# Kernel tuning notes

Measured on AMD Instinct MI355X. Metric: run time of the kernel, lower is better.

Reference implementation:

```python
import jax, jax.numpy as jnp
import numpy as np

B, N, F_IN, F_OUT, K = 128, 400, 128, 128, 5


def setup_inputs() -> dict:
    key = jax.random.key(0)
    ks = jax.random.split(key, 7)
    s_in = 1.0 / np.sqrt(F_IN)
    s_out = 1.0 / np.sqrt(F_OUT)
    return {
        "x": jax.random.normal(ks[0], (B, N, F_IN), dtype=jnp.float32),
        # SAGEConv layer 1: lin_l (neighbor agg, with bias) and lin_r (root, no bias)
        "W1l": jax.random.normal(ks[1], (F_OUT, F_IN), dtype=jnp.float32) * s_in,
        "b1l": jnp.zeros((F_OUT,), dtype=jnp.float32),
        "W1r": jax.random.normal(ks[2], (F_OUT, F_IN), dtype=jnp.float32) * s_in,
        # SAGEConv layer 2
        "W2l": jax.random.normal(ks[3], (F_OUT, F_OUT), dtype=jnp.float32) * s_out,
        "b2l": jnp.zeros((F_OUT,), dtype=jnp.float32),
        "W2r": jax.random.normal(ks[4], (F_OUT, F_OUT), dtype=jnp.float32) * s_out,
    }


def _knn_sym_adj(x):
    # x: [B, N, F]. Per-batch 5-NN graph with self-loops (loop=True),
    # then symmetrized (to_undirected coalesces duplicates -> 0/1 adjacency).
    sq = jnp.sum(x * x, axis=-1)                       # [B, N]
    d2 = sq[:, :, None] + sq[:, None, :] - 2.0 * jnp.einsum("bnd,bmd->bnm", x, x)
    _, idx = jax.lax.top_k(-d2, K)                     # [B, N, K] nearest incl. self
    A = jnp.zeros((x.shape[0], x.shape[1], x.shape[1]), dtype=x.dtype)
    bi = jnp.arange(x.shape[0])[:, None, None]
    ni = jnp.arange(x.shape[1])[None, :, None]
    A = A.at[bi, ni, idx].set(1.0)                     # A[b,i,j]=1 if j in knn(i)
    return jnp.maximum(A, A.transpose(0, 2, 1))        # undirected


def _sage(h, A, deg, Wl, bl, Wr):
    # PyG SAGEConv (mean aggr): out = lin_l(mean_j x_j) + lin_r(x_i)
    m = jnp.einsum("bnm,bmf->bnf", A, h) / deg
    return m @ Wl.T + bl + h @ Wr.T


def reference(x, W1l, b1l, W1r, W2l, b2l, W2r):
    A = _knn_sym_adj(x)
    deg = jnp.sum(A, axis=-1, keepdims=True)           # >=1 (self-loop)
    h = jax.nn.relu(_sage(x, A, deg, W1l, b1l, W1r))
    h = _sage(h, A, deg, W2l, b2l, W2r)
    return h.reshape(B * N, F_OUT)
```

## Files before the change

### kernel.cpp

```cpp
#include <hip/hip_runtime.h>
#include <hip/hip_bf16.h>
#include <stdint.h>

#define B_   128
#define N_   400
#define F_   128
#define K_   5
#define ROWS (B_ * N_)
#define POOLCAP 2048
#define DCAP 416
#define MAXFLAG ROWS
#define GAP_HEDGE 5e-4
#define DELTA_MAX 0.18f
#define NW 13
#define NCAND 24

typedef __attribute__((ext_vector_type(8))) short bf16x8;
typedef __attribute__((ext_vector_type(4))) float f32x4;

static __device__ __forceinline__ unsigned short f2bf(float f) {
  union { float f; unsigned u; } v; v.f = f;
  unsigned r = v.u + 0x7fff + ((v.u >> 16) & 1);
  return (unsigned short)(r >> 16);
}
static __device__ __forceinline__ float bf2f(unsigned short h) {
  union { unsigned u; float f; } v; v.u = ((unsigned)h) << 16; return v.f;
}

template<int M, typename T>
static __device__ __forceinline__ void insM(T d, int j, T bd[], int bj[]) {
  if (d < bd[M - 1] || (d == bd[M - 1] && j < bj[M - 1])) {
    bd[M - 1] = d; bj[M - 1] = j;
#pragma unroll
    for (int q = M - 1; q > 0; --q) {
      bool sw = (bd[q] < bd[q - 1]) || (bd[q] == bd[q - 1] && bj[q] < bj[q - 1]);
      T td = bd[q]; int tj = bj[q];
      if (sw) { bd[q] = bd[q - 1]; bd[q - 1] = td; bj[q] = bj[q - 1]; bj[q - 1] = tj; }
    }
  }
}

__global__ __launch_bounds__(256) void k_prep_rows(const float* __restrict__ x,
                                                   unsigned short* __restrict__ Y,
                                                   float* __restrict__ sq) {
  int wave = threadIdx.x >> 6, lane = threadIdx.x & 63;
  int row = blockIdx.x * 4 + wave;
  float2 v = *(const float2*)&x[(size_t)row * F_ + lane * 2];
  unsigned short hx = f2bf(v.x), hy = f2bf(v.y);
  float lx = v.x - bf2f(hx), ly = v.y - bf2f(hy);
  *(unsigned*)&Y[(size_t)row * 256 + lane * 2]       = (unsigned)hx | ((unsigned)hy << 16);
  *(unsigned*)&Y[(size_t)row * 256 + 128 + lane * 2] = (unsigned)f2bf(lx) | ((unsigned)f2bf(ly) << 16);
  float s = v.x * v.x + v.y * v.y;
#pragma unroll
  for (int o = 32; o > 0; o >>= 1) s += __shfl_xor(s, o);
  if (lane == 0) sq[row] = s;
}

__global__ __launch_bounds__(256) void k_prep_w(const float* __restrict__ W1l,
                                                const float* __restrict__ W1r,
                                                const float* __restrict__ W2l,
                                                const float* __restrict__ W2r,
                                                unsigned short* __restrict__ Wh,
                                                unsigned short* __restrict__ Wlo) {
  int t = blockIdx.x * 256 + threadIdx.x;
  int m = t >> 14, e = t & 16383;
  const float* src = (m == 0) ? W1l : (m == 1) ? W1r : (m == 2) ? W2l : W2r;
  float f = src[e];
  unsigned short h = f2bf(f);
  Wh[t] = h;
  Wlo[t] = f2bf(f - bf2f(h));
}

#define YJ_STRIDE 264
__global__ __launch_bounds__(256) void k_knn(const unsigned short* __restrict__ Y,
                                             const float* __restrict__ sq,
                                             int* __restrict__ idxout,
                                             int* __restrict__ flagcnt,
                                             int* __restrict__ flagrows,
                                             int* __restrict__ cand) {
  __shared__ unsigned short Yj[64 * YJ_STRIDE];
  __shared__ float sqj[64];

  int b = blockIdx.y, i0 = blockIdx.x * 64;
  int tid = threadIdx.x, wave = tid >> 6, lane = tid & 63;

  int i_local = wave * 16 + (lane & 15);
  int arow = b * N_ + min(i0 + i_local, N_ - 1);
  float sqi = sq[arow];

  const bf16x8* abase = (const bf16x8*)&Y[(size_t)arow * 256];
  bf16x8 af[8];
#pragma unroll
  for (int kc = 0; kc < 8; ++kc) af[kc] = abase[kc * 4 + (lane >> 4)];

  float bd[6] = {3.4e38f, 3.4e38f, 3.4e38f, 3.4e38f, 3.4e38f, 3.4e38f};
  int   bj[6] = {1 << 30, 1 << 30, 1 << 30, 1 << 30, 1 << 30, 1 << 30};

  const float4* srcb = (const float4*)(Y + (size_t)b * N_ * 256);

  for (int jt = 0; jt < 7; ++jt) {
    int j0 = jt * 64;
    float4* dst4 = (float4*)Yj;
#pragma unroll
    for (int q = 0; q < 8; ++q) {
      int l = tid + 256 * q;
      int r = l >> 5, cc = l & 31;
      int jr = min(j0 + r, N_ - 1);
      dst4[r * 33 + cc] = srcb[jr * 32 + cc];
    }
    if (tid < 64) sqj[tid] = sq[b * N_ + min(j0 + tid, N_ - 1)];
    __syncthreads();

#pragma unroll
    for (int ct = 0; ct < 4; ++ct) {
      f32x4 acc = {0.f, 0.f, 0.f, 0.f};
      int jfr = ct * 16 + (lane & 15);
      const bf16x8* bbase = (const bf16x8*)&Yj[jfr * YJ_STRIDE];
#pragma unroll
      for (int kc = 0; kc < 12; ++kc) {
        int bidx = (kc & 3) * 4 + ((kc >= 8) ? 16 : 0) + (lane >> 4);
        acc = __builtin_amdgcn_mfma_f32_16x16x32_bf16(bbase[bidx], af[kc & 7], acc, 0, 0, 0);
      }
      int jbase = ct * 16 + (lane >> 4) * 4;
      float4 sjv = *(const float4*)&sqj[jbase];
      float sj4[4] = {sjv.x, sjv.y, sjv.z, sjv.w};
#pragma unroll
      for (int r = 0; r < 4; ++r) {
        int j = j0 + jbase + r;
        float d = sqi + sj4[r] - 2.0f * acc[r];
        if (j < N_) insM<6, float>(d, j, bd, bj);
      }
    }
    __syncthreads();
  }

  float* mbd = (float*)Yj;
  int*   mbj = (int*)Yj + 64 * 33;
  int slot = i_local * 33 + (lane >> 4) * 6;
#pragma unroll
  for (int q = 0; q < 6; ++q) { mbd[slot + q] = bd[q]; mbj[slot + q] = bj[q]; }
  __syncthreads();

  if (tid < 64) {
    int i = i0 + tid;
    if (i < N_) {
      float fd[6] = {3.4e38f, 3.4e38f, 3.4e38f, 3.4e38f, 3.4e38f, 3.4e38f};
      int   fj[6] = {1 << 30, 1 << 30, 1 << 30, 1 << 30, 1 << 30, 1 << 30};
      for (int q = 0; q < NCAND; ++q)
        insM<6, float>(mbd[tid * 33 + q], mbj[tid * 33 + q], fd, fj);
      int gi = b * N_ + i;
#pragma unroll
      for (int q = 0; q < 5; ++q) idxout[gi * K_ + q] = fj[q];
      if (fd[5] - fd[4] < 0.02f) {
        int pos = atomicAdd(flagcnt, 1);
        if (pos < MAXFLAG) {
          flagrows[pos] = gi;
          for (int q = 0; q < NCAND; ++q) cand[gi * 32 + q] = mbj[tid * 33 + q];
        }
      }
    }
  }
}

__global__ __launch_bounds__(256) void k_refine(const float* __restrict__ x,
                                                const int* __restrict__ flagrows,
                                                const int* __restrict__ flagcnt,
                                                const int* __restrict__ cand,
                                                int* __restrict__ idx,
                                                int* __restrict__ hcnt,
                                                int* __restrict__ hrows,
                                                int* __restrict__ hab) {
  __shared__ double dbuf[8][32];
  __shared__ int    jbuf[8][32];
  int slot = threadIdx.x >> 5, c = threadIdx.x & 31;
  int nflag = min(*flagcnt, MAXFLAG);
  for (int base = blockIdx.x * 8; base < nflag; base += gridDim.x * 8) {
    int t = base + slot;
    __syncthreads();
    if (t < nflag) {
      if (c < NCAND) {
        int row = flagrows[t];
        int b = row / N_;
        int j = cand[row * 32 + c];
        const float* xi = x + (size_t)row * F_;
        const float* xj = x + (size_t)(b * N_ + j) * F_;
        double s = 0.0;
#pragma unroll
        for (int q = 0; q < 128; ++q) {
          double d = (double)xi[q] - (double)xj[q];
          s = fma(d, d, s);
        }
        dbuf[slot][c] = s; jbuf[slot][c] = j;
      } else {
        dbuf[slot][c] = 1e300; jbuf[slot][c] = 1 << 30;
      }
    }
    __syncthreads();
    if (c == 0 && t < nflag) {
      int row = flagrows[t];
      int b = row / N_;
      double fd[6] = {1e300, 1e300, 1e300, 1e300, 1e300, 1e300};
      int    fj[6] = {1 << 30, 1 << 30, 1 << 30, 1 << 30, 1 << 30, 1 << 30};
      for (int q = 0; q < NCAND; ++q) insM<6, double>(dbuf[slot][q], jbuf[slot][q], fd, fj);
#pragma unroll
      for (int q = 0; q < 5; ++q) idx[row * K_ + q] = fj[q];
      if (fd[5] - fd[4] < GAP_HEDGE) {
        int p = atomicAdd(hcnt, 1);
        if (p < MAXFLAG) {
          hrows[p] = row;
          hab[2 * p]     = b * N_ + fj[4];
          hab[2 * p + 1] = b * N_ + fj[5];
        }
      }
    }
  }
}

__global__ __launch_bounds__(512) void k_buildg(const int* __restrict__ idx,
                                                const int* __restrict__ c6,
                                                int* __restrict__ L6,
                                                float* __restrict__ W6,
                                                int* __restrict__ pooli,
                                                float* __restrict__ poolw,
                                                int* __restrict__ offi,
                                                int* __restrict__ cnti) {
  __shared__ unsigned bm1[N_][NW];
  __shared__ unsigned bmh[N_][NW];
  __shared__ int cs[512];
  int b = blockIdx.x, t = threadIdx.x;
  int gb0 = b * N_;

  for (int q = t; q < N_ * NW; q += 512) {
    (&bm1[0][0])[q] = 0u;
    (&bmh[0][0])[q] = 0u;
  }

  int i = t;
  int j0 = -1, j1 = -1, j2 = -1, j3 = -1, j4 = -1, y6 = -1;
  if (i < N_) {
    const int* ip = idx + (size_t)(gb0 + i) * 5;
    j0 = ip[0]; j1 = ip[1]; j2 = ip[2]; j3 = ip[3]; j4 = ip[4];
    y6 = c6[gb0 + i];
  }
  __syncthreads();

  if (i < N_) {
    unsigned bit = 1u << (i & 31);
    int w = i >> 5;
    if (j0 != i) atomicOr(&bm1[j0][w], bit);
    if (j1 != i) atomicOr(&bm1[j1][w], bit);
    if (j2 != i) atomicOr(&bm1[j2][w], bit);
    if (j3 != i) atomicOr(&bm1[j3][w], bit);
    if (j4 != i) {
      if (y6 >= 0) atomicOr(&bmh[j4][w], bit); else atomicOr(&bm1[j4][w], bit);
    }
    if (y6 >= 0 && y6 != i) atomicOr(&bmh[y6][w], bit);
  }
  __syncthreads();

  if (i < N_) {
    int gi = gb0 + i;
    int   jj[6]  = {j0, j1, j2, j3, j4, y6};
    float w1s[6] = {1.f, 1.f, 1.f, 1.f,
                    (y6 >= 0) ? 0.5f : 1.f,
                    (y6 >= 0) ? 0.5f : 0.f};
#pragma unroll
    for (int k = 0; k < 6; ++k) {
      int j = jj[k]; float w1 = w1s[k];
      size_t sl = (size_t)gi * 6 + k;
      if (w1 <= 0.f || j < 0) { L6[sl] = gi; W6[sl] = 0.f; continue; }
      if (j == i)             { L6[sl] = gi; W6[sl] = 1.f; continue; }
      float w2 = ((bm1[i][j >> 5] >> (j & 31)) & 1) ? 1.f
               : (((bmh[i][j >> 5] >> (j & 31)) & 1) ? 0.5f : 0.f);
      L6[sl] = gb0 + j; W6[sl] = fmaxf(w1, w2);
    }
  }

  unsigned mw[NW];
  int cnt_i = 0;
  if (i < N_) {
#pragma unroll
    for (int w = 0; w < NW; ++w) {
      unsigned ex = 0;
      if ((i  >> 5) == w) ex |= 1u << (i  & 31);
      if ((j0 >> 5) == w) ex |= 1u << (j0 & 31);
      if ((j1 >> 5) == w) ex |= 1u << (j1 & 31);
      if ((j2 >> 5) == w) ex |= 1u << (j2 & 31);
      if ((j3 >> 5) == w) ex |= 1u << (j3 & 31);
      if ((j4 >> 5) == w) ex |= 1u << (j4 & 31);
      if (y6 >= 0 && (y6 >> 5) == w) ex |= 1u << (y6 & 31);
      unsigned m = (bm1[i][w] | bmh[i][w]) & ~ex;
      mw[w] = m;
      cnt_i += __popc(m);
    }
  } else {
#pragma unroll
    for (int w = 0; w < NW; ++w) mw[w] = 0u;
  }

  cs[t] = (i < N_) ? cnt_i : 0;
  __syncthreads();
  for (int off = 1; off < 512; off <<= 1) {
    int v = (t >= off) ? cs[t - off] : 0;
    __syncthreads();
    cs[t] += v;
    __syncthreads();
  }

  if (i < N_) {
    int o = b * POOLCAP + cs[t] - cnt_i;
    offi[gb0 + i] = o;
    cnti[gb0 + i] = cnt_i;
    int c = 0;
#pragma unroll
    for (int w = 0; w < NW; ++w) {
      unsigned m = mw[w];
      unsigned ones = bm1[i][w];
      while (m) {
        int bit = __ffs(m) - 1; m &= m - 1;
        int r = w * 32 + bit;
        pooli[o + c] = gb0 + r;
        poolw[o + c] = ((ones >> bit) & 1) ? 1.f : 0.5f;
        ++c;
      }
    }
  }
}

__global__ __launch_bounds__(128) void k_delta(
    const float* __restrict__ P, const float* __restrict__ Qb,
    const float* __restrict__ b1, const unsigned short* __restrict__ h1b,
    const float* __restrict__ sumP, const float* __restrict__ degv,
    const int* __restrict__ L6, const float* __restrict__ W6,
    const int* __restrict__ pooli, const float* __restrict__ poolw,
    const int* __restrict__ offi, const int* __restrict__ cnti,
    const int* __restrict__ idx,
    const int* __restrict__ hcnt, const int* __restrict__ hrows,
    const int* __restrict__ hab,
    const float* __restrict__ W2l, const float* __restrict__ W2r,
    int* __restrict__ c6, int* __restrict__ dcnt, int* __restrict__ dlist) {
  __shared__ float H[3][2][128];
  __shared__ float dH[3][128];
  __shared__ float U[3][128];
  __shared__ float V1[128], V2[128], red[128];
  __shared__ float mU[3];
  __shared__ int   Ls[3][DCAP];
  __shared__ float Wsh[3][DCAP];
  int f = threadIdx.x;
  int n = min(*hcnt, MAXFLAG);
  for (int t = blockIdx.x; t < n; t += gridDim.x) {
    int gi = hrows[t], ga = hab[2 * t], gb = hab[2 * t + 1];
    int bb = gi / N_, iw = gi - bb * N_;
    bool ma = false, mb = false;
#pragma unroll
    for (int q = 0; q < K_; ++q) {
      ma = ma || (idx[ga * K_ + q] == iw);
      mb = mb || (idx[gb * K_ + q] == iw);
    }
    if (ma && mb) continue;
    int rows3[3] = {gi, ga, gb};
    int nn3[3];
    for (int s3 = 0; s3 < 3; ++s3) {
      int r = rows3[s3];
      int cc = cnti[r], oo = offi[r];
      int nn = 6 + cc; nn3[s3] = nn;
      for (int e = f; e < DCAP; e += 128) {
        int li = -1; float lw = 0.f;
        if (e < 6)      { li = L6[(size_t)r * 6 + e]; lw = W6[(size_t)r * 6 + e]; }
        else if (e < nn){ li = pooli[oo + e - 6];     lw = poolw[oo + e - 6]; }
        Ls[s3][e] = li; Wsh[s3][e] = lw;
      }
    }
    for (int s3 = 0; s3 < 3; ++s3) {
      int r = rows3[s3];
      float s1 = sumP[(size_t)r * 128 + f], d1 = degv[r];
      float ds = 0.f, dd = 0.f;
      if (s3 == 0) {
        if (!ma) { ds -= P[(size_t)ga * 128 + f]; dd -= 1.f; }
        if (!mb) { ds += P[(size_t)gb * 128 + f]; dd += 1.f; }
      } else if (s3 == 1) {
        if (!ma) { ds -= P[(size_t)gi * 128 + f]; dd -= 1.f; }
      } else {
        if (!mb) { ds += P[(size_t)gi * 128 + f]; dd += 1.f; }
      }
      float base = b1[f] + Qb[(size_t)r * 128 + f];
      float h0 = fmaxf(s1 / d1 + base, 0.f);
      float h1v = fmaxf((s1 + ds) / (d1 + dd) + base, 0.f);
      H[s3][0][f] = h0;
      H[s3][1][f] = h1v;
      dH[s3][f] = h1v - h0;
    }
    __syncthreads();
    {
      float u0 = 0.f, u1 = 0.f, u2 = 0.f;
      for (int f2 = 0; f2 < 128; ++f2) {
        float wv = W2l[f * 128 + f2];
        u0 += dH[0][f2] * wv;
        u1 += dH[1][f2] * wv;
        u2 += dH[2][f2] * wv;
      }
      U[0][f] = u0; U[1][f] = u1; U[2][f] = u2;
    }
    __syncthreads();
    red[f] = fabsf(U[0][f]);
    V1[f]  = fabsf(U[1][f]);
    V2[f]  = fabsf(U[2][f]);
    __syncthreads();
    for (int o = 64; o > 0; o >>= 1) {
      if (f < o) {
        red[f] = fmaxf(red[f], red[f + o]);
        V1[f]  = fmaxf(V1[f],  V1[f + o]);
        V2[f]  = fmaxf(V2[f],  V2[f + o]);
      }
      __syncthreads();
    }
    if (f == 0) { mU[0] = red[0]; mU[1] = V1[0]; mU[2] = V2[0]; }
    __syncthreads();
    float dmax = 0.f;
    for (int which = 0; which < 3; ++which) {
      float v1 = 0.f, v2 = 0.f;
      float d1r = degv[rows3[which]], d2r = d1r;
      int nnw = nn3[which];
      for (int e2 = 0; e2 < nnw; ++e2) {
        float w = Wsh[which][e2];
        if (w == 0.f) continue;
        int s = Ls[which][e2];
        float hv1, hv2;
        if (s == gi)      { hv1 = H[0][0][f]; hv2 = H[0][1][f]; }
        else if (s == ga) { hv1 = H[1][0][f]; hv2 = H[1][1][f]; }
        else if (s == gb) { hv1 = H[2][0][f]; hv2 = H[2][1][f]; }
        else {
          float hh = bf2f(h1b[(size_t)s * 256 + f]) + bf2f(h1b[(size_t)s * 256 + 128 + f]);
          hv1 = hh; hv2 = hh;
        }
        bool inG2 = true;
        if (which == 0 && s == ga && !ma) inG2 = false;
        if (which == 1 && s == gi && !ma) inG2 = false;
        v1 += w * hv1;
        if (inG2) v2 += w * hv2; else d2r -= w;
      }
      if (which == 0 && !mb) { v2 += H[2][1][f]; d2r += 1.f; }
      if (which == 2 && !mb) { v2 += H[0][1][f]; d2r += 1.f; }
      V1[f] = v1; V2[f] = v2;
      __syncthreads();
      float a1 = 0.f, a2 = 0.f, ow = 0.f;
      for (int f2 = 0; f2 < 128; ++f2) {
        float wl = W2l[f * 128 + f2];
        a1 += V1[f2] * wl;
        a2 += V2[f2] * wl;
        ow += dH[which][f2] * W2r[f * 128 + f2];
      }
      dmax = fmaxf(dmax, fabsf(a2 / d2r - a1 / d1r + ow));
      __syncthreads();
    }
    for (int li = 0; li < 3; ++li) {
      for (int e = f; e < nn3[li]; e += 128) {
        float w = Wsh[li][e];
        if (w == 0.f) continue;
        int r = Ls[li][e];
        if (r == gi || r == ga || r == gb) continue;
        bool dup = false;
        for (int lj = 0; lj < li && !dup; ++lj)
          for (int e2 = 0; e2 < nn3[lj]; ++e2)
            if (Ls[lj][e2] == r && Wsh[lj][e2] != 0.f) { dup = true; break; }
        if (dup) continue;
        float wi = 0.f, wa = 0.f, wb = 0.f;
        if (li == 0) wi = w; else if (li == 1) wa = w; else wb = w;
        int nz = 1;
        for (int lj = li + 1; lj < 3; ++lj)
          for (int e2 = 0; e2 < nn3[lj]; ++e2)
            if (Ls[lj][e2] == r && Wsh[lj][e2] != 0.f) {
              if (lj == 1) { if (wa == 0.f) ++nz; wa = Wsh[lj][e2]; }
              else         { if (wb == 0.f) ++nz; wb = Wsh[lj][e2]; }
            }
        float lm;
        if (nz == 1) {
          lm = (li == 0) ? wi * mU[0] : (li == 1) ? wa * mU[1] : wb * mU[2];
        } else {
          lm = 0.f;
          for (int ff = 0; ff < 128; ++ff)
            lm = fmaxf(lm, fabsf(wi * U[0][ff] + wa * U[1][ff] + wb * U[2][ff]));
        }
        dmax = fmaxf(dmax, lm / degv[r]);
      }
    }
    red[f] = dmax;
    __syncthreads();
    for (int o = 64; o > 0; o >>= 1) {
      if (f < o) red[f] = fmaxf(red[f], red[f + o]);
      __syncthreads();
    }
    if (f == 0 && red[0] < DELTA_MAX) {
      c6[gi] = gb - bb * N_;
      int p = atomicAdd(dcnt, 3);
      dlist[p] = gi; dlist[p + 1] = ga; dlist[p + 2] = gb;
    }
    __syncthreads();
  }
}

#define WSTR 130
__global__ __launch_bounds__(256) void k_gemm(const unsigned short* __restrict__ A,
                                              const unsigned short* __restrict__ Whl,
                                              const unsigned short* __restrict__ Whr,
                                              const unsigned short* __restrict__ Wll,
                                              const unsigned short* __restrict__ Wlr,
                                              float* __restrict__ P, float* __restrict__ Q) {
  __shared__ unsigned short W[2 * 128 * WSTR];
  int tid = threadIdx.x, wave = tid >> 6, lane = tid & 63;

  size_t row = (size_t)blockIdx.x * 64 + wave * 16 + (lane & 15);
  bf16x8 af[8];
#pragma unroll
  for (int s = 0; s < 2; ++s)
#pragma unroll
    for (int kc = 0; kc < 4; ++kc)
      af[s * 4 + kc] = *(const bf16x8*)&A[row * 256 + s * 128 + kc * 32 + (lane >> 4) * 8];

  size_t orow0 = (size_t)blockIdx.x * 64 + wave * 16 + (lane >> 4) * 4;
#pragma unroll
  for (int w = 0; w < 2; ++w) {
    {
      int mat = tid >> 7, nrow = tid & 127;
      const unsigned short* src =
          (mat == 0) ? ((w == 0) ? Whl : Whr) + nrow * 128
                     : ((w == 0) ? Wll : Wlr) + nrow * 128;
      unsigned short* dst = &W[(size_t)tid * WSTR];
      if (w) __syncthreads();
#pragma unroll
      for (int p = 0; p < 16; ++p) *(bf16x8*)(dst + p * 8) = *(const bf16x8*)(src + p * 8);
    }
    __syncthreads();

    float* O = w ? Q : P;
#pragma unroll
    for (int ct = 0; ct < 8; ++ct) {
      f32x4 acc = {0.f, 0.f, 0.f, 0.f};
      int n = ct * 16 + (lane & 15);
      const unsigned short* bh = &W[(size_t)n * WSTR];
      const unsigned short* bl = &W[(size_t)(128 + n) * WSTR];
#pragma unroll
      for (int kc = 0; kc < 4; ++kc) {
        bf16x8 fh = *(const bf16x8*)(bh + kc * 32 + (lane >> 4) * 8);
        bf16x8 fl_ = *(const bf16x8*)(bl + kc * 32 + (lane >> 4) * 8);
        acc = __builtin_amdgcn_mfma_f32_16x16x32_bf16(af[kc], fh, acc, 0, 0, 0);
        acc = __builtin_amdgcn_mfma_f32_16x16x32_bf16(af[4 + kc], fh, acc, 0, 0, 0);
        acc = __builtin_amdgcn_mfma_f32_16x16x32_bf16(af[kc], fl_, acc, 0, 0, 0);
      }
#pragma unroll
      for (int r = 0; r < 4; ++r)
        O[(orow0 + r) * 128 + ct * 16 + (lane & 15)] = acc[r];
    }
  }
}

__global__ __launch_bounds__(256) void k_gemm_d(const unsigned short* __restrict__ A,
                                                const unsigned short* __restrict__ Whl,
                                                const unsigned short* __restrict__ Whr,
                                                const unsigned short* __restrict__ Wll,
                                                const unsigned short* __restrict__ Wlr,
                                                float* __restrict__ P, float* __restrict__ Q,
                                                const int* __restrict__ dcnt,
                                                const int* __restrict__ dlist) {
  int dn = *dcnt;
  if (blockIdx.x * 64 >= dn) return;
  __shared__ unsigned short W[4 * 128 * WSTR];
  int tid = threadIdx.x, wave = tid >> 6, lane = tid & 63;
#pragma unroll
  for (int q = 0; q < 2; ++q) {
    int ridx = tid * 2 + q;
    int mat = ridx >> 7, n = ridx & 127;
    const unsigned short* src =
        ((mat == 0) ? Whl : (mat == 1) ? Whr : (mat == 2) ? Wll : Wlr) + n * 128;
    unsigned short* dst = &W[(size_t)ridx * WSTR];
#pragma unroll
    for (int p = 0; p < 16; ++p) *(bf16x8*)(dst + p * 8) = *(const bf16x8*)(src + p * 8);
  }
  __syncthreads();

  for (int tb = blockIdx.x * 64; tb < dn; tb += gridDim.x * 64) {
    size_t row = (size_t)dlist[min(tb + wave * 16 + (lane & 15), dn - 1)];
    bf16x8 af[8];
#pragma unroll
    for (int s = 0; s < 2; ++s)
#pragma unroll
      for (int kc = 0; kc < 4; ++kc)
        af[s * 4 + kc] = *(const bf16x8*)&A[row * 256 + s * 128 + kc * 32 + (lane >> 4) * 8];

    int lo0 = tb + wave * 16 + (lane >> 4) * 4;
#pragma unroll
    for (int w = 0; w < 2; ++w) {
      float* O = w ? Q : P;
#pragma unroll
      for (int ct = 0; ct < 8; ++ct) {
        f32x4 acc = {0.f, 0.f, 0.f, 0.f};
        int n = ct * 16 + (lane & 15);
        const unsigned short* bh = &W[(size_t)(w * 128 + n) * WSTR];
        const unsigned short* bl = &W[(size_t)((2 + w) * 128 + n) * WSTR];
#pragma unroll
        for (int kc = 0; kc < 4; ++kc) {
          bf16x8 fh = *(const bf16x8*)(bh + kc * 32 + (lane >> 4) * 8);
          bf16x8 fl_ = *(const bf16x8*)(bl + kc * 32 + (lane >> 4) * 8);
          acc = __builtin_amdgcn_mfma_f32_16x16x32_bf16(af[kc], fh, acc, 0, 0, 0);
          acc = __builtin_amdgcn_mfma_f32_16x16x32_bf16(af[4 + kc], fh, acc, 0, 0, 0);
          acc = __builtin_amdgcn_mfma_f32_16x16x32_bf16(af[kc], fl_, acc, 0, 0, 0);
        }
#pragma unroll
        for (int r = 0; r < 4; ++r) {
          size_t orow = (size_t)dlist[min(lo0 + r, dn - 1)];
          O[orow * 128 + ct * 16 + (lane & 15)] = acc[r];
        }
      }
    }
  }
}

__global__ __launch_bounds__(256) void k_aggr(const float* __restrict__ P,
                                              const float* __restrict__ Q,
                                              const int* __restrict__ L6,
                                              const float* __restrict__ W6,
                                              const int* __restrict__ pooli,
                                              const float* __restrict__ poolw,
                                              const int* __restrict__ offi,
                                              const int* __restrict__ cnti,
                                              const float* __restrict__ bias,
                                              float* __restrict__ outf,
                                              unsigned short* __restrict__ outb,
                                              float* __restrict__ sumP,
                                              float* __restrict__ degv,
                                              int relu) {
  int bid = blockIdx.x;
  int chunk = (bid & 7) * (gridDim.x >> 3) + (bid >> 3);
  int r = chunk * 8 + (threadIdx.x >> 5);
  int l4 = threadIdx.x & 31;
  int m = cnti[r], o = offi[r];
  float4 acc = {0.f, 0.f, 0.f, 0.f};
  float deg = 0.f;
#pragma unroll
  for (int k = 0; k < 6; ++k) {
    float ww = W6[(size_t)r * 6 + k];
    float4 p4 = *(const float4*)&P[(size_t)L6[(size_t)r * 6 + k] * 128 + l4 * 4];
    acc.x += ww * p4.x; acc.y += ww * p4.y;
    acc.z += ww * p4.z; acc.w += ww * p4.w;
    deg += ww;
  }
  for (int q = 0; q < m; ++q) {
    float ww = poolw[o + q];
    float4 p4 = *(const float4*)&P[(size_t)pooli[o + q] * 128 + l4 * 4];
    acc.x += ww * p4.x; acc.y += ww * p4.y;
    acc.z += ww * p4.z; acc.w += ww * p4.w;
    deg += ww;
  }
  if (sumP) {
    *(float4*)&sumP[(size_t)r * 128 + l4 * 4] = acc;
    if (l4 == 0) degv[r] = deg;
  }
  float4 b4 = *(const float4*)&bias[l4 * 4];
  float4 q4 = *(const float4*)&Q[(size_t)r * 128 + l4 * 4];
  float4 v;
  v.x = acc.x / deg + b4.x + q4.x;
  v.y = acc.y / deg + b4.y + q4.y;
  v.z = acc.z / deg + b4.z + q4.z;
  v.w = acc.w / deg + b4.w + q4.w;
  if (relu) {
    v.x = fmaxf(v.x, 0.f); v.y = fmaxf(v.y, 0.f);
    v.z = fmaxf(v.z, 0.f); v.w = fmaxf(v.w, 0.f);
  }
  if (outf) {
    *(float4*)&outf[(size_t)r * 128 + l4 * 4] = v;
  } else {
    ushort4 hi, lo;
    hi.x = f2bf(v.x); hi.y = f2bf(v.y); hi.z = f2bf(v.z); hi.w = f2bf(v.w);
    lo.x = f2bf(v.x - bf2f(hi.x)); lo.y = f2bf(v.y - bf2f(hi.y));
    lo.z = f2bf(v.z - bf2f(hi.z)); lo.w = f2bf(v.w - bf2f(hi.w));
    *(ushort4*)&outb[(size_t)r * 256 + l4 * 4] = hi;
    *(ushort4*)&outb[(size_t)r * 256 + 128 + l4 * 4] = lo;
  }
}

__global__ __launch_bounds__(256) void k_aggr_d(const float* __restrict__ P,
                                                const float* __restrict__ Q,
                                                const int* __restrict__ L6,
                                                const float* __restrict__ W6,
                                                const int* __restrict__ pooli,
                                                const float* __restrict__ poolw,
                                                const int* __restrict__ offi,
                                                const int* __restrict__ cnti,
                                                const float* __restrict__ bias,
                                                unsigned short* __restrict__ outb,
                                                const int* __restrict__ dcnt,
                                                const int* __restrict__ dlist) {
  int dn = *dcnt;
  int l4 = threadIdx.x & 31;
  for (int di = blockIdx.x * 8 + (threadIdx.x >> 5); di < dn; di += gridDim.x * 8) {
    int r = dlist[di];
    int m = cnti[r], o = offi[r];
    float4 acc = {0.f, 0.f, 0.f, 0.f};
    float deg = 0.f;
#pragma unroll
    for (int k = 0; k < 6; ++k) {
      float ww = W6[(size_t)r * 6 + k];
      float4 p4 = *(const float4*)&P[(size_t)L6[(size_t)r * 6 + k] * 128 + l4 * 4];
      acc.x += ww * p4.x; acc.y += ww * p4.y;
      acc.z += ww * p4.z; acc.w += ww * p4.w;
      deg += ww;
    }
    for (int q = 0; q < m; ++q) {
      float ww = poolw[o + q];
      float4 p4 = *(const float4*)&P[(size_t)pooli[o + q] * 128 + l4 * 4];
      acc.x += ww * p4.x; acc.y += ww * p4.y;
      acc.z += ww * p4.z; acc.w += ww * p4.w;
      deg += ww;
    }
    float4 b4 = *(const float4*)&bias[l4 * 4];
    float4 q4 = *(const float4*)&Q[(size_t)r * 128 + l4 * 4];
    float4 v;
    v.x = fmaxf(acc.x / deg + b4.x + q4.x, 0.f);
    v.y = fmaxf(acc.y / deg + b4.y + q4.y, 0.f);
    v.z = fmaxf(acc.z / deg + b4.z + q4.z, 0.f);
    v.w = fmaxf(acc.w / deg + b4.w + q4.w, 0.f);
    ushort4 hi, lo;
    hi.x = f2bf(v.x); hi.y = f2bf(v.y); hi.z = f2bf(v.z); hi.w = f2bf(v.w);
    lo.x = f2bf(v.x - bf2f(hi.x)); lo.y = f2bf(v.y - bf2f(hi.y));
    lo.z = f2bf(v.z - bf2f(hi.z)); lo.w = f2bf(v.w - bf2f(hi.w));
    *(ushort4*)&outb[(size_t)r * 256 + l4 * 4] = hi;
    *(ushort4*)&outb[(size_t)r * 256 + 128 + l4 * 4] = lo;
  }
}

extern "C" void kernel_launch(void* const* d_in, const int* in_sizes, int n_in,
                              void* d_out, int out_size, void* d_ws, size_t ws_size,
                              hipStream_t stream) {
  const float* x   = (const float*)d_in[0];
  const float* W1l = (const float*)d_in[1];
  const float* b1l = (const float*)d_in[2];
  const float* W1r = (const float*)d_in[3];
  const float* W2l = (const float*)d_in[4];
  const float* b2l = (const float*)d_in[5];
  const float* W2r = (const float*)d_in[6];
  float* out = (float*)d_out;

  char* w = (char*)d_ws;
  unsigned short* Y    = (unsigned short*)w; w += (size_t)ROWS * 256 * 2;
  float*          sq   = (float*)w;          w += (size_t)ROWS * 4;
  unsigned short* Wh   = (unsigned short*)w; w += (size_t)4 * 16384 * 2;
  unsigned short* Wlo  = (unsigned short*)w; w += (size_t)4 * 16384 * 2;
  int*            idx  = (int*)w;            w += (size_t)ROWS * K_ * 4;
  int*            L6   = (int*)w;            w += (size_t)ROWS * 6 * 4;
  float*          W6   = (float*)w;          w += (size_t)ROWS * 6 * 4;
  int*            pooli= (int*)w;            w += (size_t)B_ * POOLCAP * 4;
  float*          poolw= (float*)w;          w += (size_t)B_ * POOLCAP * 4;
  int*            offi = (int*)w;            w += (size_t)ROWS * 4;
  int*            cnti = (int*)w;            w += (size_t)ROWS * 4;
  int*            flags = (int*)w;           w += 64;
  int*            c6   = (int*)w;            w += (size_t)ROWS * 4;
  int*            dlist= (int*)w;            w += (size_t)3 * MAXFLAG * 4;
  int*            flagrows = (int*)w;        w += (size_t)MAXFLAG * 4;
  int*            hrows = (int*)w;           w += (size_t)MAXFLAG * 4;
  int*            hab  = (int*)w;            w += (size_t)MAXFLAG * 8;
  int*            candb = (int*)w;           w += (size_t)ROWS * 32 * 4;
  float*          P    = (float*)w;          w += (size_t)ROWS * 128 * 4;
  float*          Qb   = (float*)w;          w += (size_t)ROWS * 128 * 4;
  unsigned short* h1b  = (unsigned short*)w; w += (size_t)ROWS * 256 * 2;
  float*          sumP = (float*)w;          w += (size_t)ROWS * 128 * 4;
  float*          degv = (float*)w;          w += (size_t)ROWS * 4;
  float* P2 = (float*)Y;
  float* Q2 = sumP;
  (void)ws_size; (void)in_sizes; (void)n_in; (void)out_size;

  hipMemsetAsync(flags, 0, 64, stream);
  hipMemsetAsync(c6, 0xFF, (size_t)ROWS * 4, stream);
  k_prep_rows<<<ROWS / 4, 256, 0, stream>>>(x, Y, sq);
  k_prep_w<<<(4 * 16384) / 256, 256, 0, stream>>>(W1l, W1r, W2l, W2r, Wh, Wlo);
  k_knn<<<dim3(7, B_), 256, 0, stream>>>(Y, sq, idx, &flags[0], flagrows, candb);
  k_gemm<<<ROWS / 64, 256, 0, stream>>>(Y, Wh, Wh + 16384, Wlo, Wlo + 16384, P, Qb);
  k_refine<<<64, 256, 0, stream>>>(x, flagrows, &flags[0], candb, idx,
                                   &flags[1], hrows, hab);
  k_buildg<<<B_, 512, 0, stream>>>(idx, c6, L6, W6, pooli, poolw, offi, cnti);
  k_aggr<<<ROWS / 8, 256, 0, stream>>>(P, Qb, L6, W6, pooli, poolw, offi, cnti,
                                       b1l, nullptr, h1b, sumP, degv, 1);
  k_delta<<<512, 128, 0, stream>>>(P, Qb, b1l, h1b, sumP, degv, L6, W6, pooli,
                                   poolw, offi, cnti, idx, &flags[1], hrows, hab,
                                   W2l, W2r, c6, &flags[2], dlist);
  k_buildg<<<B_, 512, 0, stream>>>(idx, c6, L6, W6, pooli, poolw, offi, cnti);
  k_gemm<<<ROWS / 64, 256, 0, stream>>>(h1b, Wh + 2 * 16384, Wh + 3 * 16384,
                                        Wlo + 2 * 16384, Wlo + 3 * 16384, P2, Q2);
  k_aggr_d<<<64, 256, 0, stream>>>(P, Qb, L6, W6, pooli, poolw, offi, cnti,
                                   b1l, h1b, &flags[2], dlist);
  k_gemm_d<<<32, 256, 0, stream>>>(h1b, Wh + 2 * 16384, Wh + 3 * 16384,
                                   Wlo + 2 * 16384, Wlo + 3 * 16384, P2, Q2,
                                   &flags[2], dlist);
  k_aggr<<<ROWS / 8, 256, 0, stream>>>(P2, Q2, L6, W6, pooli, poolw, offi, cnti,
                                       b2l, out, nullptr, nullptr, nullptr, 0);
}
```

Before: 586.6 us.

## Split KNN column range across two blocks and merge partial top-6 lists

The KNN kernel now splits the 7 column tiles into two halves along a new grid z dimension, doubling the block count. Each half writes a per-row top-6 list to scratch, and a new merge kernel combines them, writes the indices and flags near-tie rows. The refine candidate count drops from 24 to 12 (the two merged top-6 lists), and the refine grid grows from 64 to 256 blocks. The cost is an extra launch plus scratch traffic, and near-tie refinement now sees fewer candidates, which could miss a true neighbour.

```diff
diff --git a/kernel.cpp b/kernel.cpp
--- a/kernel.cpp
+++ b/kernel.cpp
@@ -13,7 +13,7 @@
 #define GAP_HEDGE 5e-4
 #define DELTA_MAX 0.18f
 #define NW 13
-#define NCAND 24
+#define NCAND 12
 
 typedef __attribute__((ext_vector_type(8))) short bf16x8;
 typedef __attribute__((ext_vector_type(4))) float f32x4;
@@ -74,14 +74,12 @@
 #define YJ_STRIDE 264
 __global__ __launch_bounds__(256) void k_knn(const unsigned short* __restrict__ Y,
                                              const float* __restrict__ sq,
-                                             int* __restrict__ idxout,
-                                             int* __restrict__ flagcnt,
-                                             int* __restrict__ flagrows,
-                                             int* __restrict__ cand) {
+                                             float* __restrict__ halfd,
+                                             int* __restrict__ halfj) {
   __shared__ unsigned short Yj[64 * YJ_STRIDE];
   __shared__ float sqj[64];
 
-  int b = blockIdx.y, i0 = blockIdx.x * 64;
+  int b = blockIdx.y, i0 = blockIdx.x * 64, half = blockIdx.z;
   int tid = threadIdx.x, wave = tid >> 6, lane = tid & 63;
 
   int i_local = wave * 16 + (lane & 15);
@@ -98,7 +96,8 @@
 
   const float4* srcb = (const float4*)(Y + (size_t)b * N_ * 256);
 
-  for (int jt = 0; jt < 7; ++jt) {
+  int jt0 = half * 4, jt1 = half ? 7 : 4;
+  for (int jt = jt0; jt < jt1; ++jt) {
     int j0 = jt * 64;
     float4* dst4 = (float4*)Yj;
 #pragma unroll
@@ -146,18 +145,37 @@
     if (i < N_) {
       float fd[6] = {3.4e38f, 3.4e38f, 3.4e38f, 3.4e38f, 3.4e38f, 3.4e38f};
       int   fj[6] = {1 << 30, 1 << 30, 1 << 30, 1 << 30, 1 << 30, 1 << 30};
-      for (int q = 0; q < NCAND; ++q)
+      for (int q = 0; q < 24; ++q)
         insM<6, float>(mbd[tid * 33 + q], mbj[tid * 33 + q], fd, fj);
-      int gi = b * N_ + i;
-#pragma unroll
-      for (int q = 0; q < 5; ++q) idxout[gi * K_ + q] = fj[q];
-      if (fd[5] - fd[4] < 0.02f) {
-        int pos = atomicAdd(flagcnt, 1);
-        if (pos < MAXFLAG) {
-          flagrows[pos] = gi;
-          for (int q = 0; q < NCAND; ++q) cand[gi * 32 + q] = mbj[tid * 33 + q];
-        }
-      }
+      size_t gi = (size_t)(b * N_ + i);
+#pragma unroll
+      for (int q = 0; q < 6; ++q) {
+        halfd[gi * 12 + half * 6 + q] = fd[q];
+        halfj[gi * 12 + half * 6 + q] = fj[q];
+      }
+    }
+  }
+}
+
+__global__ __launch_bounds__(256) void k_kmerge(const float* __restrict__ halfd,
+                                                const int* __restrict__ halfj,
+                                                int* __restrict__ idxout,
+                                                int* __restrict__ flagcnt,
+                                                int* __restrict__ flagrows,
+                                                int* __restrict__ cand) {
+  size_t r = (size_t)blockIdx.x * 256 + threadIdx.x;
+  float fd[6] = {3.4e38f, 3.4e38f, 3.4e38f, 3.4e38f, 3.4e38f, 3.4e38f};
+  int   fj[6] = {1 << 30, 1 << 30, 1 << 30, 1 << 30, 1 << 30, 1 << 30};
+#pragma unroll
+  for (int q = 0; q < 12; ++q)
+    insM<6, float>(halfd[r * 12 + q], halfj[r * 12 + q], fd, fj);
+#pragma unroll
+  for (int q = 0; q < 5; ++q) idxout[r * K_ + q] = fj[q];
+  if (fd[5] - fd[4] < 0.02f) {
+    int pos = atomicAdd(flagcnt, 1);
+    if (pos < MAXFLAG) {
+      flagrows[pos] = (int)r;
+      for (int q = 0; q < 12; ++q) cand[r * 32 + q] = halfj[r * 12 + q];
     }
   }
 }
@@ -181,7 +199,7 @@
       if (c < NCAND) {
         int row = flagrows[t];
         int b = row / N_;
-        int j = cand[row * 32 + c];
+        int j = cand[(size_t)row * 32 + c];
         const float* xi = x + (size_t)row * F_;
         const float* xj = x + (size_t)(b * N_ + j) * F_;
         double s = 0.0;
@@ -759,6 +777,8 @@
   int*            hrows = (int*)w;           w += (size_t)MAXFLAG * 4;
   int*            hab  = (int*)w;            w += (size_t)MAXFLAG * 8;
   int*            candb = (int*)w;           w += (size_t)ROWS * 32 * 4;
+  float*          halfdb = (float*)w;        w += (size_t)ROWS * 12 * 4;
+  int*            halfjb = (int*)w;          w += (size_t)ROWS * 12 * 4;
   float*          P    = (float*)w;          w += (size_t)ROWS * 128 * 4;
   float*          Qb   = (float*)w;          w += (size_t)ROWS * 128 * 4;
   unsigned short* h1b  = (unsigned short*)w; w += (size_t)ROWS * 256 * 2;
@@ -772,10 +792,12 @@
   hipMemsetAsync(c6, 0xFF, (size_t)ROWS * 4, stream);
   k_prep_rows<<<ROWS / 4, 256, 0, stream>>>(x, Y, sq);
   k_prep_w<<<(4 * 16384) / 256, 256, 0, stream>>>(W1l, W1r, W2l, W2r, Wh, Wlo);
-  k_knn<<<dim3(7, B_), 256, 0, stream>>>(Y, sq, idx, &flags[0], flagrows, candb);
+  k_knn<<<dim3(7, B_, 2), 256, 0, stream>>>(Y, sq, halfdb, halfjb);
+  k_kmerge<<<ROWS / 256, 256, 0, stream>>>(halfdb, halfjb, idx, &flags[0],
+                                           flagrows, candb);
   k_gemm<<<ROWS / 64, 256, 0, stream>>>(Y, Wh, Wh + 16384, Wlo, Wlo + 16384, P, Qb);
-  k_refine<<<64, 256, 0, stream>>>(x, flagrows, &flags[0], candb, idx,
-                                   &flags[1], hrows, hab);
+  k_refine<<<256, 256, 0, stream>>>(x, flagrows, &flags[0], candb, idx,
+                                    &flags[1], hrows, hab);
   k_buildg<<<B_, 512, 0, stream>>>(idx, c6, L6, W6, pooli, poolw, offi, cnti);
   k_aggr<<<ROWS / 8, 256, 0, stream>>>(P, Qb, L6, W6, pooli, poolw, offi, cnti,
                                        b1l, nullptr, h1b, sumP, degv, 1);
```

Result: no change. 582.5 us (median of 2 runs) (-0.7%).
